# Optimization experiments

Measured on AMD Instinct MI355X. Metric: run time of the kernel, lower is better.

## Reference

```python
import jax, jax.numpy as jnp
import numpy as np

L, D, F, H = 6, 512, 2048, 8
DH = D // H
SCALE = DH ** -0.5
B, S = 2, 2048


def _ln(x, w, b):
    m = jnp.mean(x, axis=-1, keepdims=True)
    v = jnp.var(x, axis=-1, keepdims=True)
    return (x - m) * jax.lax.rsqrt(v + 1e-5) * w + b


def setup_inputs() -> dict:
    key = jax.random.key(0)
    ks = jax.random.split(key, 10)
    s = 0.02
    return {
        "x": jax.random.normal(ks[0], (B, S, D), jnp.float32),
        "mask": jnp.zeros((B, 1, 1, S), jnp.float32),
        "ln1_w": jnp.ones((L, D), jnp.float32),
        "ln1_b": jnp.zeros((L, D), jnp.float32),
        "in_w": s * jax.random.normal(ks[1], (L, D, 3 * D), jnp.float32),
        "in_b": jnp.zeros((L, 3 * D), jnp.float32),
        "out_w": s * jax.random.normal(ks[2], (L, D, D), jnp.float32),
        "out_b": jnp.zeros((L, D), jnp.float32),
        "ln2_w": jnp.ones((L, D), jnp.float32),
        "ln2_b": jnp.zeros((L, D), jnp.float32),
        "ffn1_w": s * jax.random.normal(ks[3], (L, D, F), jnp.float32),
        "ffn1_b": jnp.zeros((L, F), jnp.float32),
        "ffn2_w": s * jax.random.normal(ks[4], (L, F, D), jnp.float32),
        "ffn2_b": jnp.zeros((L, D), jnp.float32),
        "norm_w": jnp.ones((D,), jnp.float32),
        "norm_b": jnp.zeros((D,), jnp.float32),
    }


def reference(x, mask, ln1_w, ln1_b, in_w, in_b, out_w, out_b,
              ln2_w, ln2_b, ffn1_w, ffn1_b, ffn2_w, ffn2_b, norm_w, norm_b):
    def step(h, p):
        (l1w, l1b, iw, ib, ow, ob, l2w, l2b, f1w, f1b, f2w, f2b) = p
        # --- self-attention (pre-norm) ---
        y = _ln(h, l1w, l1b)
        proj = y @ iw + ib                       # [B,S,3D]
        q, k, v = jnp.split(proj, 3, axis=-1)    # each [B,S,D]
        q = q.reshape(B, S, H, DH)
        k = k.reshape(B, S, H, DH)
        v = v.reshape(B, S, H, DH)
        dot = jnp.einsum('bqhd,bkhd->bhqk', q * SCALE, k) + mask  # [B,H,S,S]
        att = jax.nn.softmax(dot, axis=-1)
        o = jnp.einsum('bhqk,bkhd->bqhd', att, v).reshape(B, S, D)
        h = o @ ow + ob + h
        # --- FFN (pre-norm) ---
        y = _ln(h, l2w, l2b)
        y = jax.nn.relu(y @ f1w + f1b) @ f2w + f2b
        return h + y, None

    params = (ln1_w, ln1_b, in_w, in_b, out_w, out_b,
              ln2_w, ln2_b, ffn1_w, ffn1_b, ffn2_w, ffn2_b)
    x, _ = jax.lax.scan(step, x, params)
    return _ln(x, norm_w, norm_b)
```

## Files before the change

### kernel.cpp

```cpp
#include <hip/hip_runtime.h>
#include <hip/hip_bf16.h>
#include <stdint.h>


typedef __bf16 bf16x8 __attribute__((ext_vector_type(8)));
typedef __bf16 bf16x4 __attribute__((ext_vector_type(4)));
typedef float f32x4 __attribute__((ext_vector_type(4)));
typedef float f32x16 __attribute__((ext_vector_type(16)));
typedef unsigned short u16;
typedef unsigned short u16x8 __attribute__((ext_vector_type(8)));

#define NB 2
#define NS 2048
#define ND 512
#define NH 8
#define NDH 64
#define NF 2048
#define NL 6
#define NCHUNK 4
#define CK (NS / NCHUNK)
#define LOG2E 1.4426950408889634f
#define QSCALE (0.125f * LOG2E)

#if defined(__has_builtin)
#if __has_builtin(__builtin_amdgcn_global_load_lds)
#define HAVE_GLDS 1
#endif
#endif
#ifndef HAVE_GLDS
#define HAVE_GLDS 0
#endif

#if HAVE_GLDS
__device__ __forceinline__ void glds16(const u16* g, u16* l) {
  __builtin_amdgcn_global_load_lds(
      (const __attribute__((address_space(1))) unsigned int*)g,
      (__attribute__((address_space(3))) unsigned int*)l, 16, 0, 0);
}
#endif

__device__ __forceinline__ u16 f2bf(float f) {
  unsigned u = __float_as_uint(f);
  u += 0x7FFFu + ((u >> 16) & 1u);
  return (u16)(u >> 16);
}

__device__ __forceinline__ int xswz(int w, int n) {
  return (w & 7) * (n >> 3) + (w >> 3);
}

__global__ __launch_bounds__(256) void wcvt_t(const float* __restrict__ src,
                                              u16* __restrict__ dst,
                                              int K, int N) {
  __shared__ float tile[32][33];
  int l = blockIdx.z;
  const float* s = src + (size_t)l * K * N;
  u16* d = dst + (size_t)l * K * N;
  int k0 = blockIdx.y * 32, n0 = blockIdx.x * 32;
  int tx = threadIdx.x, ty = threadIdx.y;
  for (int i = 0; i < 32; i += 8)
    tile[ty + i][tx] = s[(size_t)(k0 + ty + i) * N + n0 + tx];
  __syncthreads();
  for (int i = 0; i < 32; i += 8)
    d[(size_t)(n0 + ty + i) * K + k0 + tx] = f2bf(tile[tx][ty + i]);
}

template <int OUT_BF16>
__global__ __launch_bounds__(256) void ln_k(const float* __restrict__ x,
                                            const float* __restrict__ w,
                                            const float* __restrict__ b,
                                            void* __restrict__ out) {
  int row = blockIdx.x;
  int t = threadIdx.x;
  const float* xr = x + (size_t)row * ND;
  float2 v = ((const float2*)xr)[t];
  float s = v.x + v.y, ss = v.x * v.x + v.y * v.y;
  for (int o = 32; o > 0; o >>= 1) {
    s += __shfl_down(s, o);
    ss += __shfl_down(ss, o);
  }
  __shared__ float rs[4], rss[4];
  if ((t & 63) == 0) { rs[t >> 6] = s; rss[t >> 6] = ss; }
  __syncthreads();
  float S = rs[0] + rs[1] + rs[2] + rs[3];
  float SS = rss[0] + rss[1] + rss[2] + rss[3];
  float mean = S * (1.0f / ND);
  float var = SS * (1.0f / ND) - mean * mean;
  float rstd = rsqrtf(var + 1e-5f);
  float2 wv = ((const float2*)w)[t];
  float2 bv = ((const float2*)b)[t];
  float y0 = (v.x - mean) * rstd * wv.x + bv.x;
  float y1 = (v.y - mean) * rstd * wv.y + bv.y;
  if (OUT_BF16) {
    ushort2 p; p.x = f2bf(y0); p.y = f2bf(y1);
    ((ushort2*)out)[(size_t)row * (ND / 2) + t] = p;
  } else {
    float2 p; p.x = y0; p.y = y1;
    ((float2*)out)[(size_t)row * (ND / 2) + t] = p;
  }
}

template <int EPI, int BM, int BN, int BK>
__device__ __forceinline__ void gemm_body(int flat, int gx, int gy,
                                          const u16* __restrict__ A,
                                          const u16* __restrict__ Bt,
                                          const float* __restrict__ bias,
                                          const float* __restrict__ resid,
                                          void* __restrict__ C,
                                          int M, int N, int K, int lda,
                                          u16* sm) {
  constexpr int MT = BM / 32;
  constexpr int NT = BN / 32;
  constexpr int CB = BK / 8;
  constexpr int RPP = 2048 / BK;
  constexpr int AP = BM / RPP;
  constexpr int BP = BN / RPP;
  constexpr int KK = BK / 32;
  constexpr int LAU = BM * BK;
  constexpr int LBU = BN * BK;
  int s_id = xswz(flat, gx * gy);
  int bn = s_id % gx, bm = s_id / gx;
  int t = threadIdx.x;
  int wave = t >> 6, lane = t & 63, quad = lane >> 4, l15 = lane & 15;
  int wm = (wave >> 1) * (BM / 2), wn = (wave & 1) * (BN / 2);
  f32x4 acc[MT][NT] = {};
  int srow = t / CB;
  int scol = ((t % CB) ^ (srow & (CB - 1))) * 8;
  const u16* Ag = A + (size_t)(bm * BM) * lda;
  const u16* Bg = Bt + (size_t)(bn * BN) * lda;

  auto stage = [&](int k0, int buf) {
    u16* laB = sm + buf * LAU;
    u16* lbB = sm + 2 * LAU + buf * LBU;
#if HAVE_GLDS
    u16* laW = laB + wave * 512;
    u16* lbW = lbB + wave * 512;
#pragma unroll
    for (int g = 0; g < AP; g++)
      glds16(&Ag[(size_t)(srow + g * RPP) * lda + k0 + scol], laW + g * 2048);
#pragma unroll
    for (int g = 0; g < BP; g++)
      glds16(&Bg[(size_t)(srow + g * RPP) * lda + k0 + scol], lbW + g * 2048);
#else
#pragma unroll
    for (int g = 0; g < AP; g++)
      *(bf16x8*)&laB[(srow + g * RPP) * BK + (t % CB) * 8] =
          *(const bf16x8*)&Ag[(size_t)(srow + g * RPP) * lda + k0 + scol];
#pragma unroll
    for (int g = 0; g < BP; g++)
      *(bf16x8*)&lbB[(srow + g * RPP) * BK + (t % CB) * 8] =
          *(const bf16x8*)&Bg[(size_t)(srow + g * RPP) * lda + k0 + scol];
#endif
  };

  stage(0, 0);
  const int nk = K / BK;
  int cur = 0;
  for (int ks = 0; ks < nk; ks++) {
    __syncthreads();
    if (ks + 1 < nk) stage((ks + 1) * BK, cur ^ 1);
    const u16* lac = sm + cur * LAU;
    const u16* lbc = sm + 2 * LAU + cur * LBU;
#pragma unroll
    for (int kk = 0; kk < KK; kk++) {
      bf16x8 af[MT], bfr[NT];
#pragma unroll
      for (int i = 0; i < MT; i++) {
        int row = wm + i * 16 + l15;
        af[i] = *(const bf16x8*)&lac[row * BK + ((kk * 4 + quad) ^ (row & (CB - 1))) * 8];
      }
#pragma unroll
      for (int i = 0; i < NT; i++) {
        int row = wn + i * 16 + l15;
        bfr[i] = *(const bf16x8*)&lbc[row * BK + ((kk * 4 + quad) ^ (row & (CB - 1))) * 8];
      }
#pragma unroll
      for (int mt = 0; mt < MT; mt++)
#pragma unroll
        for (int nt = 0; nt < NT; nt++)
          acc[mt][nt] = __builtin_amdgcn_mfma_f32_16x16x32_bf16(
              af[mt], bfr[nt], acc[mt][nt], 0, 0, 0);
    }
    cur ^= 1;
  }
#pragma unroll
  for (int mt = 0; mt < MT; mt++)
#pragma unroll
    for (int nt = 0; nt < NT; nt++) {
      int col = bn * BN + wn + nt * 16 + l15;
      float bcol = (EPI == 3) ? 0.f : bias[col];
#pragma unroll
      for (int r = 0; r < 4; r++) {
        int row = bm * BM + wm + mt * 16 + quad * 4 + r;
        float v = acc[mt][nt][r] + ((EPI == 3) ? bias[row] : bcol);
        if (EPI == 1) v = fmaxf(v, 0.f);
        if (EPI == 2)
          ((float*)C)[(size_t)row * N + col] = v + resid[(size_t)row * N + col];
        else
          ((u16*)C)[(size_t)row * N + col] = f2bf(v);
      }
    }
}

template <int EPI, int BM, int BN, int BK>
__global__ __launch_bounds__(256) void gemm_bt(const u16* __restrict__ A,
                                               const u16* __restrict__ Bt,
                                               const float* __restrict__ bias,
                                               const float* __restrict__ resid,
                                               void* __restrict__ C,
                                               int M, int N, int K, int lda) {
  __shared__ __align__(16) u16 sm[2 * BM * BK + 2 * BN * BK];
  int flat = blockIdx.x + gridDim.x * blockIdx.y;
  gemm_body<EPI, BM, BN, BK>(flat, gridDim.x, gridDim.y, A, Bt, bias, resid,
                             C, M, N, K, lda, sm);
}

__global__ __launch_bounds__(256) void qkv_k(const u16* __restrict__ ybuf,
                                             const u16* __restrict__ wq_l,
                                             const float* __restrict__ inb_l,
                                             u16* __restrict__ qk,
                                             u16* __restrict__ vtb) {
  __shared__ __align__(16) u16 sm[32768];
  int f = blockIdx.x;
  if (f < 512) {
    gemm_body<0, 64, 128, 64>(f, 2 * ND / 128, NB * NS / 64, ybuf, wq_l,
                              inb_l, nullptr, qk, NB * NS, 2 * ND, ND, ND, sm);
  } else {
    gemm_body<3, 64, 64, 128>(f - 512, NB * NS / 64, ND / 64,
                              wq_l + (size_t)2 * ND * ND, ybuf,
                              inb_l + 2 * ND, nullptr, vtb, ND, NB * NS, ND,
                              ND, sm);
  }
}

__global__ __launch_bounds__(256) void attn_k(const u16* __restrict__ qk,
                                              const u16* __restrict__ vt,
                                              const float* __restrict__ mask,
                                              u16* __restrict__ opart,
                                              float* __restrict__ lbuf) {
  __shared__ u16 kt_s[64 * 64];
  __shared__ u16 vt_s[64 * 64];
  __shared__ float mask_s[CK];
  int flat = blockIdx.x + 16 * (blockIdx.y + 16 * blockIdx.z);
  int s_id = xswz(flat, 16 * 16 * NCHUNK);
  int qt = s_id & 15;
  int bh = (s_id >> 4) & 15;
  int c = s_id >> 8;
  int b = bh >> 3, h = bh & 7;
  int t = threadIdx.x;
  int wave = t >> 6, lane = t & 63, l31 = lane & 31, H = lane >> 5;
  bool H0 = (H == 0);

  {
    const float* mrow = mask + b * NS + c * CK;
    mask_s[t] = mrow[t] * LOG2E;
    mask_s[t + 256] = mrow[t + 256] * LOG2E;
  }

  int qrow = qt * 128 + wave * 32 + l31;
  const u16* qbase = qk + ((size_t)(b * NS + qrow)) * (2 * ND) + h * NDH;
  bf16x8 qf[4];
#pragma unroll
  for (int kk = 0; kk < 4; kk++) {
    qf[kk] = *(const bf16x8*)&qbase[kk * 16 + H * 8];
#pragma unroll
    for (int e = 0; e < 8; e++) qf[kk][e] = (__bf16)((float)qf[kk][e] * QSCALE);
  }

  f32x16 oacc[2] = {};
  float lhalf = 0.f;

  int srow8 = t >> 3;
  int segsw = ((t & 7) ^ ((t >> 3) & 7)) * 8;
  const u16* kg0 = qk + ((size_t)(b * NS + srow8)) * (2 * ND) + ND + h * NDH + segsw;
  const u16* vg0 = vt + ((size_t)(h * NDH + srow8)) * (NB * NS) + b * NS + segsw;
#if HAVE_GLDS
  u16* ktB = kt_s + wave * 512;
  u16* vtB = vt_s + wave * 512;
#endif
  for (int kt0 = c * CK; kt0 < (c + 1) * CK; kt0 += 64) {
    __syncthreads();
#if HAVE_GLDS
    glds16(&kg0[(size_t)kt0 * (2 * ND)], ktB);
    glds16(&kg0[(size_t)(kt0 + 32) * (2 * ND)], ktB + 2048);
    glds16(&vg0[kt0], vtB);
    glds16(&vg0[kt0 + (size_t)32 * (NB * NS)], vtB + 2048);
#else
    *(bf16x8*)&kt_s[srow8 * 64 + (t & 7) * 8] =
        *(const bf16x8*)&kg0[(size_t)kt0 * (2 * ND)];
    *(bf16x8*)&kt_s[(srow8 + 32) * 64 + (t & 7) * 8] =
        *(const bf16x8*)&kg0[(size_t)(kt0 + 32) * (2 * ND)];
    *(bf16x8*)&vt_s[srow8 * 64 + (t & 7) * 8] = *(const bf16x8*)&vg0[kt0];
    *(bf16x8*)&vt_s[(srow8 + 32) * 64 + (t & 7) * 8] =
        *(const bf16x8*)&vg0[kt0 + (size_t)32 * (NB * NS)];
#endif
    __syncthreads();
    int ktl = kt0 - c * CK;
    f32x16 sc[2];
#pragma unroll
    for (int kt = 0; kt < 2; kt++) {
#pragma unroll
      for (int g = 0; g < 4; g++) {
        f32x4 mm = *(const f32x4*)&mask_s[ktl + 32 * kt + 8 * g + 4 * H];
#pragma unroll
        for (int e = 0; e < 4; e++) sc[kt][4 * g + e] = mm[e];
      }
      int row = 32 * kt + l31;
#pragma unroll
      for (int kk = 0; kk < 4; kk++) {
        bf16x8 kf = *(const bf16x8*)&kt_s[row * 64 + (((2 * kk + H) ^ (row & 7)) << 3)];
        sc[kt] = __builtin_amdgcn_mfma_f32_32x32x16_bf16(kf, qf[kk], sc[kt], 0, 0, 0);
      }
    }
    unsigned p2[2][4][2];
#pragma unroll
    for (int kt = 0; kt < 2; kt++)
#pragma unroll
      for (int r2 = 0; r2 < 4; r2++)
#pragma unroll
        for (int p = 0; p < 2; p++) {
          float e0 = __builtin_amdgcn_exp2f(sc[kt][4 * r2 + 2 * p]);
          float e1 = __builtin_amdgcn_exp2f(sc[kt][4 * r2 + 2 * p + 1]);
          lhalf += e0 + e1;
          float2 pp; pp.x = e0; pp.y = e1;
          __hip_bfloat162 bb = __float22bfloat162_rn(pp);
          p2[kt][r2][p] = *reinterpret_cast<unsigned*>(&bb);
        }
    bf16x8 pfk[4];
#pragma unroll
    for (int kk = 0; kk < 4; kk++) {
      const int kt = kk >> 1;
      const int b0 = 2 * (kk & 1), b1 = b0 + 1;
      unsigned sent0 = H0 ? p2[kt][b1][0] : p2[kt][b0][0];
      unsigned sent1 = H0 ? p2[kt][b1][1] : p2[kt][b0][1];
      unsigned r0 = (unsigned)__shfl_xor((int)sent0, 32);
      unsigned r1 = (unsigned)__shfl_xor((int)sent1, 32);
      uint4 pk;
      pk.x = H0 ? p2[kt][b0][0] : r0;
      pk.y = H0 ? p2[kt][b0][1] : r1;
      pk.z = H0 ? r0 : p2[kt][b1][0];
      pk.w = H0 ? r1 : p2[kt][b1][1];
      pfk[kk] = *reinterpret_cast<bf16x8*>(&pk);
    }
#pragma unroll
    for (int dt = 0; dt < 2; dt++) {
      int row = dt * 32 + l31;
#pragma unroll
      for (int kk = 0; kk < 4; kk++) {
        bf16x8 vf = *(const bf16x8*)&vt_s[row * 64 + (((2 * kk + H) ^ (row & 7)) << 3)];
        oacc[dt] = __builtin_amdgcn_mfma_f32_32x32x16_bf16(pfk[kk], vf, oacc[dt], 0, 0, 0);
      }
    }
  }
  float lsum = lhalf + (float)__shfl_xor((float)lhalf, 32);
  u16* ob = opart + (((size_t)(c * NB * NH + bh) * NS) + qt * 128 + wave * 32) * NDH;
#pragma unroll
  for (int dt = 0; dt < 2; dt++)
#pragma unroll
    for (int r = 0; r < 16; r++) {
      int q = (r & 3) + 8 * (r >> 2) + 4 * H;
      ob[(size_t)q * NDH + dt * 32 + l31] = f2bf(oacc[dt][r]);
    }
  if (H == 0) {
    size_t li = (size_t)(c * NB * NH + bh) * NS + qt * 128 + wave * 32 + l31;
    lbuf[li] = lsum;
  }
}

__global__ __launch_bounds__(256) void attn_merge(const u16* __restrict__ opart,
                                                  const float* __restrict__ lbuf,
                                                  u16* __restrict__ o) {
  int gt = blockIdx.x * 256 + threadIdx.x;
  int grp = gt & 7;
  int s = (gt >> 3) & (NS - 1);
  int bh = gt >> 14;
  float L = 0.f;
#pragma unroll
  for (int c = 0; c < NCHUNK; c++)
    L += lbuf[(size_t)(c * NB * NH + bh) * NS + s];
  float inv = 1.0f / L;
  float acc[8] = {};
#pragma unroll
  for (int c = 0; c < NCHUNK; c++) {
    bf16x8 ov = *(const bf16x8*)&opart[((size_t)(c * NB * NH + bh) * NS + s) * NDH + grp * 8];
#pragma unroll
    for (int j = 0; j < 8; j++) acc[j] += (float)ov[j];
  }
  u16x8 res;
#pragma unroll
  for (int j = 0; j < 8; j++) res[j] = f2bf(acc[j] * inv);
  int b = bh >> 3, h = bh & 7;
  *(u16x8*)&o[((size_t)(b * NS + s)) * ND + h * NDH + grp * 8] = res;
}

extern "C" void kernel_launch(void* const* d_in, const int* in_sizes, int n_in,
                              void* d_out, int out_size, void* d_ws, size_t ws_size,
                              hipStream_t stream) {
  const float* x = (const float*)d_in[0];
  const float* mask = (const float*)d_in[1];
  const float* ln1w = (const float*)d_in[2];
  const float* ln1b = (const float*)d_in[3];
  const float* in_w = (const float*)d_in[4];
  const float* in_b = (const float*)d_in[5];
  const float* out_w = (const float*)d_in[6];
  const float* out_b = (const float*)d_in[7];
  const float* ln2w = (const float*)d_in[8];
  const float* ln2b = (const float*)d_in[9];
  const float* f1w = (const float*)d_in[10];
  const float* f1b = (const float*)d_in[11];
  const float* f2w = (const float*)d_in[12];
  const float* f2b = (const float*)d_in[13];
  const float* normw = (const float*)d_in[14];
  const float* normb = (const float*)d_in[15];

  char* ws = (char*)d_ws;
  auto carve = [&](size_t bytes) {
    char* p = ws;
    ws += (bytes + 255) & ~(size_t)255;
    return p;
  };
  u16* wq_t = (u16*)carve((size_t)NL * 3 * ND * ND * 2);
  u16* wo_t = (u16*)carve((size_t)NL * ND * ND * 2);
  u16* w1_t = (u16*)carve((size_t)NL * NF * ND * 2);
  u16* w2_t = (u16*)carve((size_t)NL * ND * NF * 2);
  u16* ybuf = (u16*)carve((size_t)NB * NS * ND * 2);
  u16* qk = (u16*)carve((size_t)NB * NS * 2 * ND * 2);
  u16* vtb = (u16*)carve((size_t)ND * NB * NS * 2);
  u16* obuf = (u16*)carve((size_t)NB * NS * ND * 2);
  u16* ubuf = (u16*)carve((size_t)NB * NS * NF * 2);
  float* hA = (float*)carve((size_t)NB * NS * ND * 4);
  float* hB = (float*)carve((size_t)NB * NS * ND * 4);
  float* lbuf = (float*)carve((size_t)NCHUNK * NB * NH * NS * 4);
  u16* opart = ubuf;

  const int M = NB * NS;
  dim3 tb(32, 8);
  wcvt_t<<<dim3(3 * ND / 32, ND / 32, NL), tb, 0, stream>>>(in_w, wq_t, ND, 3 * ND);
  wcvt_t<<<dim3(ND / 32, ND / 32, NL), tb, 0, stream>>>(out_w, wo_t, ND, ND);
  wcvt_t<<<dim3(NF / 32, ND / 32, NL), tb, 0, stream>>>(f1w, w1_t, ND, NF);
  wcvt_t<<<dim3(ND / 32, NF / 32, NL), tb, 0, stream>>>(f2w, w2_t, NF, ND);

  const float* hin = x;
  for (int l = 0; l < NL; l++) {
    ln_k<1><<<M, 256, 0, stream>>>(hin, ln1w + l * ND, ln1b + l * ND, ybuf);
    qkv_k<<<1024, 256, 0, stream>>>(ybuf, wq_t + (size_t)l * 3 * ND * ND,
                                    in_b + (size_t)l * 3 * ND, qk, vtb);
    attn_k<<<dim3(NS / 128, NB * NH, NCHUNK), 256, 0, stream>>>(
        qk, vtb, mask, opart, lbuf);
    attn_merge<<<(NB * NH * NS * 8) / 256, 256, 0, stream>>>(opart, lbuf, obuf);
    gemm_bt<2, 64, 64, 128><<<dim3(ND / 64, M / 64), 256, 0, stream>>>(
        obuf, wo_t + (size_t)l * ND * ND, out_b + l * ND, hin, hB, M, ND, ND, ND);
    ln_k<1><<<M, 256, 0, stream>>>(hB, ln2w + l * ND, ln2b + l * ND, ybuf);
    gemm_bt<1, 128, 128, 64><<<dim3(NF / 128, M / 128), 256, 0, stream>>>(
        ybuf, w1_t + (size_t)l * NF * ND, f1b + l * NF, nullptr, ubuf,
        M, NF, ND, ND);
    gemm_bt<2, 64, 64, 128><<<dim3(ND / 64, M / 64), 256, 0, stream>>>(
        ubuf, w2_t + (size_t)l * ND * NF, f2b + l * ND, hB, hA, M, ND, NF, NF);
    hin = hA;
  }
  ln_k<0><<<M, 256, 0, stream>>>(hA, normw, normb, (float*)d_out);
}
```

Measured before the change: 708.5 us.

## Split K across two wave groups in out-proj and FFN2 GEMMs

Adds a gemm_sk kernel with 512 threads per block, where two halves of the block each compute half of the K reduction into separate double-buffered LDS arenas and then combine partial sums through shared memory before applying bias and residual. It replaces the 64x64 gemm_bt used for the attention output projection and the second FFN GEMM. The aim is more waves per output tile to hide latency on these narrow-N GEMMs (N=512), which launch only 512 blocks. In exchange it doubles LDS per block, adds an LDS reduction step, and uses a smaller BK.

```diff
diff --git a/kernel.cpp b/kernel.cpp
--- a/kernel.cpp
+++ b/kernel.cpp
@@ -215,6 +215,120 @@
                              C, M, N, K, lda, sm);
 }
 
+template <int BM, int BN, int BK>
+__global__ __launch_bounds__(512) void gemm_sk(const u16* __restrict__ A,
+                                               const u16* __restrict__ Bt,
+                                               const float* __restrict__ bias,
+                                               const float* __restrict__ resid,
+                                               float* __restrict__ C,
+                                               int M, int N, int K, int lda) {
+  constexpr int CB = BK / 8;
+  constexpr int KK = BK / 32;
+  constexpr int LAU = BM * BK;
+  constexpr int LBU = BN * BK;
+  constexpr int ARENA = 2 * LAU + 2 * LBU;
+  __shared__ __align__(16) u16 sm[2 * ARENA];
+  int flat = blockIdx.x + gridDim.x * blockIdx.y;
+  int s_id = xswz(flat, gridDim.x * gridDim.y);
+  int bn = s_id % gridDim.x, bm = s_id / gridDim.x;
+  int t = threadIdx.x;
+  int wave = t >> 6, lane = t & 63, quad = lane >> 4, l15 = lane & 15;
+  int half = wave >> 2, w4 = wave & 3;
+  int t256 = t & 255;
+  int wm = (w4 >> 1) * (BM / 2), wn = (w4 & 1) * (BN / 2);
+  u16* smh = sm + half * ARENA;
+  f32x4 acc[2][2] = {};
+  int srow = t256 / CB;
+  int scol = ((t256 % CB) ^ (srow & (CB - 1))) * 8;
+  const u16* Ag = A + (size_t)(bm * BM) * lda + half * (K / 2);
+  const u16* Bg = Bt + (size_t)(bn * BN) * lda + half * (K / 2);
+
+  auto stage = [&](int k0, int buf) {
+    u16* laB = smh + buf * LAU;
+    u16* lbB = smh + 2 * LAU + buf * LBU;
+#if HAVE_GLDS
+    u16* laW = laB + w4 * 512;
+    u16* lbW = lbB + w4 * 512;
+#pragma unroll
+    for (int g = 0; g < BM / 32; g++)
+      glds16(&Ag[(size_t)(srow + g * 32) * lda + k0 + scol], laW + g * 2048);
+#pragma unroll
+    for (int g = 0; g < BN / 32; g++)
+      glds16(&Bg[(size_t)(srow + g * 32) * lda + k0 + scol], lbW + g * 2048);
+#else
+#pragma unroll
+    for (int g = 0; g < BM / 32; g++)
+      *(bf16x8*)&laB[(srow + g * 32) * BK + (t256 % CB) * 8] =
+          *(const bf16x8*)&Ag[(size_t)(srow + g * 32) * lda + k0 + scol];
+#pragma unroll
+    for (int g = 0; g < BN / 32; g++)
+      *(bf16x8*)&lbB[(srow + g * 32) * BK + (t256 % CB) * 8] =
+          *(const bf16x8*)&Bg[(size_t)(srow + g * 32) * lda + k0 + scol];
+#endif
+  };
+
+  stage(0, 0);
+  const int nk = (K / 2) / BK;
+  int cur = 0;
+  for (int ks = 0; ks < nk; ks++) {
+    __syncthreads();
+    if (ks + 1 < nk) stage((ks + 1) * BK, cur ^ 1);
+    const u16* lac = smh + cur * LAU;
+    const u16* lbc = smh + 2 * LAU + cur * LBU;
+#pragma unroll
+    for (int kk = 0; kk < KK; kk++) {
+      bf16x8 af[2], bfr[2];
+#pragma unroll
+      for (int i = 0; i < 2; i++) {
+        int row = wm + i * 16 + l15;
+        af[i] = *(const bf16x8*)&lac[row * BK + ((kk * 4 + quad) ^ (row & (CB - 1))) * 8];
+      }
+#pragma unroll
+      for (int i = 0; i < 2; i++) {
+        int row = wn + i * 16 + l15;
+        bfr[i] = *(const bf16x8*)&lbc[row * BK + ((kk * 4 + quad) ^ (row & (CB - 1))) * 8];
+      }
+#pragma unroll
+      for (int mt = 0; mt < 2; mt++)
+#pragma unroll
+        for (int nt = 0; nt < 2; nt++)
+          acc[mt][nt] = __builtin_amdgcn_mfma_f32_16x16x32_bf16(
+              af[mt], bfr[nt], acc[mt][nt], 0, 0, 0);
+    }
+    cur ^= 1;
+  }
+  __syncthreads();
+  float* red = (float*)sm;
+  if (half == 1) {
+#pragma unroll
+    for (int mt = 0; mt < 2; mt++)
+#pragma unroll
+      for (int nt = 0; nt < 2; nt++)
+#pragma unroll
+        for (int r = 0; r < 4; r++)
+          red[(wm + mt * 16 + quad * 4 + r) * BN + wn + nt * 16 + l15] =
+              acc[mt][nt][r];
+  }
+  __syncthreads();
+  if (half == 0) {
+#pragma unroll
+    for (int mt = 0; mt < 2; mt++)
+#pragma unroll
+      for (int nt = 0; nt < 2; nt++) {
+        int cl = wn + nt * 16 + l15;
+        int col = bn * BN + cl;
+        float bcol = bias[col];
+#pragma unroll
+        for (int r = 0; r < 4; r++) {
+          int rl = wm + mt * 16 + quad * 4 + r;
+          int row = bm * BM + rl;
+          float v = acc[mt][nt][r] + red[rl * BN + cl] + bcol;
+          C[(size_t)row * N + col] = v + resid[(size_t)row * N + col];
+        }
+      }
+  }
+}
+
 __global__ __launch_bounds__(256) void qkv_k(const u16* __restrict__ ybuf,
                                              const u16* __restrict__ wq_l,
                                              const float* __restrict__ inb_l,
@@ -448,13 +562,13 @@
     attn_k<<<dim3(NS / 128, NB * NH, NCHUNK), 256, 0, stream>>>(
         qk, vtb, mask, opart, lbuf);
     attn_merge<<<(NB * NH * NS * 8) / 256, 256, 0, stream>>>(opart, lbuf, obuf);
-    gemm_bt<2, 64, 64, 128><<<dim3(ND / 64, M / 64), 256, 0, stream>>>(
+    gemm_sk<64, 64, 64><<<dim3(ND / 64, M / 64), 512, 0, stream>>>(
         obuf, wo_t + (size_t)l * ND * ND, out_b + l * ND, hin, hB, M, ND, ND, ND);
     ln_k<1><<<M, 256, 0, stream>>>(hB, ln2w + l * ND, ln2b + l * ND, ybuf);
     gemm_bt<1, 128, 128, 64><<<dim3(NF / 128, M / 128), 256, 0, stream>>>(
         ybuf, w1_t + (size_t)l * NF * ND, f1b + l * NF, nullptr, ubuf,
         M, NF, ND, ND);
-    gemm_bt<2, 64, 64, 128><<<dim3(ND / 64, M / 64), 256, 0, stream>>>(
+    gemm_sk<64, 64, 64><<<dim3(ND / 64, M / 64), 512, 0, stream>>>(
         ubuf, w2_t + (size_t)l * ND * NF, f2b + l * ND, hB, hA, M, ND, NF, NF);
     hin = hA;
   }
```

Measured after the change: 715.2 us. About the same (+0.9%).
